# Performance work log

Measured on AMD Instinct MI355X. Metric: run time of the kernel, lower is better.

## Reference

```python
import jax, jax.numpy as jnp
import numpy as np

MARGIN = 0.2
NEG_SENTINEL = -1e30


def setup_inputs() -> dict:
    key = jax.random.key(0)
    k1, k2 = jax.random.split(key)
    batch_reprs = jax.random.normal(k1, (4096, 128), dtype=jnp.float32)
    batch_labels = jax.random.randint(k2, (4096,), 0, 512, dtype=jnp.int64 if jax.config.jax_enable_x64 else jnp.int32)
    return {"batch_reprs": batch_reprs, "batch_labels": batch_labels}


def _loss(batch_reprs, batch_labels):
    # class match matrix (self-similarity kept, as in original)
    match = (batch_labels[:, None] == batch_labels[None, :]).astype(batch_reprs.dtype)  # [B,B]

    # pairwise euclidean distance (squared=False), sim = -dist
    sq = jnp.sum(batch_reprs * batch_reprs, axis=1)
    d2 = jnp.maximum(sq[:, None] + sq[None, :] - 2.0 * (batch_reprs @ batch_reprs.T), 0.0)
    zero = (d2 == 0.0).astype(batch_reprs.dtype)
    dist = jnp.sqrt(d2 + zero * 1e-16) * (1.0 - zero)
    sim_hat = -dist + (1.0 - match) * MARGIN  # use_margin=True

    # rank positions via double argsort (descending)
    order = jnp.argsort(-sim_hat, axis=1)
    rank = jnp.argsort(order, axis=1).astype(sim_hat.dtype) + 1.0  # [B,B], 1-based ranks

    k = jnp.sum(match, axis=1, keepdims=True)                      # n_pos per row, [B,1]
    fp = (match < 1.0) & (rank <= k)                               # false positives
    fp_num = jnp.sum(fp, axis=1, keepdims=True).astype(sim_hat.dtype)
    fn = (match > 0.0) & (rank > k)                                # false negatives

    n = sim_hat.shape[1]
    # per-row top-(fp_num) false negatives by sim_hat, vectorized via masked sort
    fn_scores = jnp.where(fn, sim_hat, NEG_SENTINEL)
    idx = jnp.argsort(-fn_scores, axis=1)
    fn_sorted = jnp.take_along_axis(sim_hat, idx, axis=1)
    fn_ranks = jnp.take_along_axis(rank, idx, axis=1)
    fn_mask_sorted = jnp.take_along_axis(fn, idx, axis=1)
    sel = (jnp.arange(n)[None, :] < fp_num) & fn_mask_sorted       # top fp_num entries

    # weighted margins (rows with fp_num==0 contribute 0 automatically)
    fp_term = jnp.sum(jnp.where(fp, sim_hat * (0.5 + (k - rank + 1.0) / k * 0.5), 0.0))
    fn_term = jnp.sum(jnp.where(sel, fn_sorted * (0.5 + (fn_ranks - k) / (n - k) * 0.5), 0.0))
    return fp_term - fn_term


def reference(batch_reprs, batch_labels):
    return _loss(batch_reprs, batch_labels)
```

## Files before the change

kernel.cpp:

```cpp
#include <hip/hip_runtime.h>
#include <cstdint>
#include <cstddef>

#define B 4096
#define D 128
#define MARGIN_F 0.2f
#define CW 256
#define ROWS 16
#define SSTR 4104

typedef short bf16x8 __attribute__((ext_vector_type(8)));
typedef float f32x4 __attribute__((ext_vector_type(4)));
typedef uint32_t u32x4 __attribute__((ext_vector_type(4)));

__device__ __forceinline__ uint32_t xform_key(float f) {
    uint32_t u = __float_as_uint(f);
    return u ^ (uint32_t)((((int32_t)u) >> 31) | 0x80000000);
}
__device__ __forceinline__ float unxform16(uint32_t k16) {
    uint32_t u = k16 << 16;
    u = (u & 0x80000000u) ? (u ^ 0x80000000u) : ~u;
    return __uint_as_float(u);
}
__device__ __forceinline__ unsigned short f2bf(float f) {
    uint32_t u = __float_as_uint(f);
    return (unsigned short)((u + 0x7FFFu + ((u >> 16) & 1u)) >> 16);
}

__global__ __launch_bounds__(256) void prep_kernel(const float* __restrict__ R,
                                                   float* __restrict__ sq,
                                                   unsigned short* __restrict__ Rb,
                                                   float* __restrict__ out) {
    if (blockIdx.x == 0 && threadIdx.x == 0) out[0] = 0.0f;
    int wave = threadIdx.x >> 6;
    int lane = threadIdx.x & 63;
    int row  = blockIdx.x * 4 + wave;
    const float2* R2 = (const float2*)R + (size_t)row * (D / 2);
    float2 v = R2[lane];
    ushort2 o; o.x = f2bf(v.x); o.y = f2bf(v.y);
    *(ushort2*)(Rb + (size_t)row * D + lane * 2) = o;
    float s = v.x * v.x + v.y * v.y;
#pragma unroll
    for (int off = 32; off > 0; off >>= 1) s += __shfl_down(s, off);
    if (lane == 0) sq[row] = s;
}

__global__ __launch_bounds__(512) void fused_loss(const unsigned short* __restrict__ Rb,
                                                  const float* __restrict__ sq,
                                                  const int* __restrict__ labels,
                                                  float* __restrict__ out) {
    __shared__ unsigned short S[ROWS * SSTR];
    __shared__ uint32_t cand_c[ROWS][CW];
    __shared__ int cnt[ROWS];

    const int tid  = threadIdx.x;
    const int wid  = tid >> 6, lane = tid & 63;
    const int q    = lane >> 4, t = lane & 15;
    const int r0   = blockIdx.x * ROWS;

    {
        uint32_t* cz = &cand_c[0][0];
#pragma unroll
        for (int c = 0; c < (ROWS * CW) / 512; ++c)
            cz[tid + c * 512] = 0u;
    }
    if (tid < ROWS) cnt[tid] = 0;

    bf16x8 af[4];
    const unsigned short* baseA = Rb + (size_t)(r0 + t) * D + q * 8;
#pragma unroll
    for (int kq = 0; kq < 4; ++kq)
        af[kq] = *(const bf16x8*)(baseA + kq * 32);

    float sqa[4]; int la[4];
#pragma unroll
    for (int rr = 0; rr < 4; ++rr) {
        sqa[rr] = sq[r0 + q * 4 + rr];
        la[rr]  = labels[r0 + q * 4 + rr];
    }

    for (int i = 0; i < 32; ++i) {
        const int jt  = wid * 32 + i;
        const int col = jt * 16 + t;
        const unsigned short* baseB = Rb + (size_t)col * D + q * 8;
        bf16x8 bfr[4];
#pragma unroll
        for (int kq = 0; kq < 4; ++kq)
            bfr[kq] = *(const bf16x8*)(baseB + kq * 32);
        f32x4 acc = (f32x4)0.0f;
#pragma unroll
        for (int kq = 0; kq < 4; ++kq)
            acc = __builtin_amdgcn_mfma_f32_16x16x32_bf16(af[kq], bfr[kq], acc, 0, 0, 0);

        const float sqc = sq[col];
        const int   lc  = labels[col];
#pragma unroll
        for (int rr = 0; rr < 4; ++rr) {
            float g  = acc[rr];
            float d2 = fmaxf(sqa[rr] + sqc - 2.0f * g, 0.0f);
            float dist = (d2 > 0.0f) ? sqrtf(d2) : 0.0f;
            float s = -dist + ((la[rr] == lc) ? 0.0f : MARGIN_F);
            uint32_t key = xform_key(s);
            S[(q * 4 + rr) * SSTR + col] = (unsigned short)((key + 0x8000u) >> 16);
        }
    }
    __syncthreads();

    float facc = 0.0f;
    const int4* lv = (const int4*)labels;

    for (int rr2 = 0; rr2 < 2; ++rr2) {
        const int row  = wid * 2 + rr2;
        const int grow = r0 + row;
        const int li   = labels[grow];

        uint64_t mbits = 0;
        uint32_t t1 = 0, t2 = 0;

        {
            u32x4 kv[8];
#pragma unroll
            for (int qq = 0; qq < 8; ++qq)
                kv[qq] = *(u32x4*)(&S[row * SSTR + (qq * 64 + lane) * 8]);

#pragma unroll
            for (int qq = 0; qq < 8; ++qq) {
                const int lb = (qq * 64 + lane) * 2;
                int4 la4 = lv[lb], lc4 = lv[lb + 1];
                uint32_t u[8] = {kv[qq].x & 0xFFFFu, kv[qq].x >> 16,
                                 kv[qq].y & 0xFFFFu, kv[qq].y >> 16,
                                 kv[qq].z & 0xFFFFu, kv[qq].z >> 16,
                                 kv[qq].w & 0xFFFFu, kv[qq].w >> 16};
#pragma unroll
                for (int c = 0; c < 8; ++c) {
                    uint32_t mn = min(t1, u[c]);
                    t1 = max(t1, u[c]);
                    t2 = max(t2, mn);
                }
                mbits |= (uint64_t)(la4.x == li) << (qq * 8 + 0);
                mbits |= (uint64_t)(la4.y == li) << (qq * 8 + 1);
                mbits |= (uint64_t)(la4.z == li) << (qq * 8 + 2);
                mbits |= (uint64_t)(la4.w == li) << (qq * 8 + 3);
                mbits |= (uint64_t)(lc4.x == li) << (qq * 8 + 4);
                mbits |= (uint64_t)(lc4.y == li) << (qq * 8 + 5);
                mbits |= (uint64_t)(lc4.z == li) << (qq * 8 + 6);
                mbits |= (uint64_t)(lc4.w == li) << (qq * 8 + 7);
            }

            int kloc = __popcll(mbits);
#pragma unroll
            for (int off = 32; off > 0; off >>= 1) kloc += __shfl_xor(kloc, off);
            const int k0 = kloc;

            const int kneed = min(k0, 128);
            uint32_t T = 0;
#pragma unroll
            for (int b = 15; b >= 0; --b) {
                uint32_t g = T | (1u << b);
                int c = __popcll(__ballot(t1 >= g)) + __popcll(__ballot(t2 >= g));
                if (c >= kneed) T = g;
            }
            t1 = T;
            t2 = (uint32_t)k0;

#pragma unroll
            for (int qq = 0; qq < 8; ++qq) {
                uint32_t u[8] = {kv[qq].x & 0xFFFFu, kv[qq].x >> 16,
                                 kv[qq].y & 0xFFFFu, kv[qq].y >> 16,
                                 kv[qq].z & 0xFFFFu, kv[qq].z >> 16,
                                 kv[qq].w & 0xFFFFu, kv[qq].w >> 16};
                int jb = (qq * 64 + lane) * 8;
#pragma unroll
                for (int c = 0; c < 8; ++c) {
                    int e = qq * 8 + c;
                    uint32_t m = (uint32_t)((mbits >> e) & 1);
                    if (u[c] >= t1 || m) {
                        int p = atomicAdd(&cnt[row], 1);
                        if (p < CW)
                            cand_c[row][p] = (u[c] << 12) | (uint32_t)(4095 - (jb + c)) | (m << 31);
                    }
                }
            }
        }

        const uint32_t T = t1;
        const int k = (int)t2;
        const float kf = (float)k;
        const uint32_t combT = T << 12;
        const int ncand = min(cnt[row], CW);

        uint32_t cr0 = cand_c[row][lane];
        uint32_t cr1 = cand_c[row][lane + 64];
        uint32_t cr2 = cand_c[row][lane + 128];
        uint32_t cr3 = cand_c[row][lane + 192];
        uint32_t mycomb[4] = {cr0 & 0x7FFFFFFFu, cr1 & 0x7FFFFFFFu,
                              cr2 & 0x7FFFFFFFu, cr3 & 0x7FFFFFFFu};
        int mym[4]  = {(int)(cr0 >> 31), (int)(cr1 >> 31),
                       (int)(cr2 >> 31), (int)(cr3 >> 31)};
        int myok[4] = {lane < ncand, lane + 64 < ncand,
                       lane + 128 < ncand, lane + 192 < ncand};
        int myc[4]  = {0, 0, 0, 0};

        const int npad = (ncand + 7) & ~7;
        for (int c0i = 0; c0i < npad; c0i += 8) {
            u32x4 a = *(const u32x4*)&cand_c[row][c0i];
            u32x4 b = *(const u32x4*)&cand_c[row][c0i + 4];
            uint32_t vv[8] = {a.x, a.y, a.z, a.w, b.x, b.y, b.z, b.w};
#pragma unroll
            for (int e = 0; e < 8; ++e) {
                uint32_t vm = vv[e] & 0x7FFFFFFFu;
#pragma unroll
                for (int j = 0; j < 4; ++j)
                    myc[j] += (vm > mycomb[j]) ? 1 : 0;
            }
        }

#pragma unroll
        for (int j = 0; j < 4; ++j) {
            if (myok[j] && mycomb[j] >= combT) {
                int rank = 1 + myc[j];
                float v = unxform16(mycomb[j] >> 12);
                if (!mym[j] && rank <= k)
                    facc += v * (0.5f + ((kf - (float)rank + 1.0f) / kf) * 0.5f);
                else if (mym[j] && rank > k)
                    facc -= v * (0.5f + (((float)rank - kf) / (float)(B - k)) * 0.5f);
            }
        }

        uint32_t p0 = 0xFFFFFFFFu, p1 = 0xFFFFFFFFu, p2 = 0xFFFFFFFFu, p3 = 0xFFFFFFFFu;

        auto flush4 = [&](int npv) {
            int c0 = 0, c1 = 0, c2 = 0, c3 = 0;
#pragma unroll
            for (int qq = 0; qq < 8; ++qq) {
                u32x4 kq = *(const u32x4*)(&S[row * SSTR + (qq * 64 + lane) * 8]);
                uint32_t u[8] = {kq.x & 0xFFFFu, kq.x >> 16,
                                 kq.y & 0xFFFFu, kq.y >> 16,
                                 kq.z & 0xFFFFu, kq.z >> 16,
                                 kq.w & 0xFFFFu, kq.w >> 16};
                int jb = (qq * 64 + lane) * 8;
#pragma unroll
                for (int cc = 0; cc < 8; ++cc) {
                    uint32_t ce = (u[cc] << 12) | (uint32_t)(4095 - (jb + cc));
                    c0 += (ce > p0) ? 1 : 0;  c1 += (ce > p1) ? 1 : 0;
                    c2 += (ce > p2) ? 1 : 0;  c3 += (ce > p3) ? 1 : 0;
                }
            }
#pragma unroll
            for (int off = 32; off > 0; off >>= 1) {
                c0 += __shfl_xor(c0, off); c1 += __shfl_xor(c1, off);
                c2 += __shfl_xor(c2, off); c3 += __shfl_xor(c3, off);
            }
            if (lane == 0) {
                if (npv > 0) facc -= unxform16(p0 >> 12) * (0.5f + (((float)(1 + c0) - kf) / (float)(B - k)) * 0.5f);
                if (npv > 1) facc -= unxform16(p1 >> 12) * (0.5f + (((float)(1 + c1) - kf) / (float)(B - k)) * 0.5f);
                if (npv > 2) facc -= unxform16(p2 >> 12) * (0.5f + (((float)(1 + c2) - kf) / (float)(B - k)) * 0.5f);
                if (npv > 3) facc -= unxform16(p3 >> 12) * (0.5f + (((float)(1 + c3) - kf) / (float)(B - k)) * 0.5f);
            }
            p0 = p1 = p2 = p3 = 0xFFFFFFFFu;
        };

        int np = 0;
#pragma unroll
        for (int j = 0; j < 4; ++j) {
            uint64_t mg = __ballot(myok[j] && mym[j] && (mycomb[j] < combT));
            while (mg) {
                int src = __ffsll((unsigned long long)mg) - 1;
                mg &= mg - 1;
                uint32_t pc;
                if (j == 0)      pc = __shfl(mycomb[0], src);
                else if (j == 1) pc = __shfl(mycomb[1], src);
                else if (j == 2) pc = __shfl(mycomb[2], src);
                else             pc = __shfl(mycomb[3], src);
                switch (np) {
                    case 0: p0 = pc; break; case 1: p1 = pc; break;
                    case 2: p2 = pc; break; default: p3 = pc; break;
                }
                ++np;
                if (np == 4) { flush4(4); np = 0; }
            }
        }
        if (np > 0) flush4(np);
    }

#pragma unroll
    for (int off = 32; off > 0; off >>= 1) facc += __shfl_xor(facc, off);
    if (lane == 0) atomicAdd(out, facc);
}

extern "C" void kernel_launch(void* const* d_in, const int* in_sizes, int n_in,
                              void* d_out, int out_size, void* d_ws, size_t ws_size,
                              hipStream_t stream) {
    const float* R      = (const float*)d_in[0];
    const int*   labels = (const int*)d_in[1];
    float* out = (float*)d_out;

    float*          sq = (float*)d_ws;
    unsigned short* Rb = (unsigned short*)((char*)d_ws + 16 * 1024);

    hipLaunchKernelGGL(prep_kernel, dim3(B / 4), dim3(256), 0, stream, R, sq, Rb, out);
    hipLaunchKernelGGL(fused_loss, dim3(B / ROWS), dim3(512), 0, stream,
                       Rb, sq, labels, out);
}
```

Baseline: 134.1 us.

## Prefetch B tiles, interleave two rows per wave, replace atomic compaction with prefix scan

The GEMM loop now software-prefetches the next column tile's bf16 fragments, squared norms and labels so their loads overlap the current MFMA and epilogue. The selection phase processes both of a wave's rows together to give more independent work per instruction. The shared-memory atomicAdd candidate compaction is replaced by a deterministic wave prefix-sum compaction. Row keys are kept in registers for the below-threshold pass instead of being reloaded from LDS, which raises register pressure and may cut occupancy.

```diff
diff --git a/kernel.cpp b/kernel.cpp
--- a/kernel.cpp
+++ b/kernel.cpp
@@ -51,7 +51,6 @@
                                                   float* __restrict__ out) {
     __shared__ unsigned short S[ROWS * SSTR];
     __shared__ uint32_t cand_c[ROWS][CW];
-    __shared__ int cnt[ROWS];
 
     const int tid  = threadIdx.x;
     const int wid  = tid >> 6, lane = tid & 63;
@@ -64,7 +63,6 @@
         for (int c = 0; c < (ROWS * CW) / 512; ++c)
             cz[tid + c * 512] = 0u;
     }
-    if (tid < ROWS) cnt[tid] = 0;
 
     bf16x8 af[4];
     const unsigned short* baseA = Rb + (size_t)(r0 + t) * D + q * 8;
@@ -79,29 +77,50 @@
         la[rr]  = labels[r0 + q * 4 + rr];
     }
 
-    for (int i = 0; i < 32; ++i) {
-        const int jt  = wid * 32 + i;
-        const int col = jt * 16 + t;
-        const unsigned short* baseB = Rb + (size_t)col * D + q * 8;
+    {
+        const int jt0 = wid * 32;
+        int col = jt0 * 16 + t;
         bf16x8 bfr[4];
-#pragma unroll
-        for (int kq = 0; kq < 4; ++kq)
-            bfr[kq] = *(const bf16x8*)(baseB + kq * 32);
-        f32x4 acc = (f32x4)0.0f;
-#pragma unroll
-        for (int kq = 0; kq < 4; ++kq)
-            acc = __builtin_amdgcn_mfma_f32_16x16x32_bf16(af[kq], bfr[kq], acc, 0, 0, 0);
-
-        const float sqc = sq[col];
-        const int   lc  = labels[col];
-#pragma unroll
-        for (int rr = 0; rr < 4; ++rr) {
-            float g  = acc[rr];
-            float d2 = fmaxf(sqa[rr] + sqc - 2.0f * g, 0.0f);
-            float dist = (d2 > 0.0f) ? sqrtf(d2) : 0.0f;
-            float s = -dist + ((la[rr] == lc) ? 0.0f : MARGIN_F);
-            uint32_t key = xform_key(s);
-            S[(q * 4 + rr) * SSTR + col] = (unsigned short)((key + 0x8000u) >> 16);
+        {
+            const unsigned short* baseB = Rb + (size_t)col * D + q * 8;
+#pragma unroll
+            for (int kq = 0; kq < 4; ++kq)
+                bfr[kq] = *(const bf16x8*)(baseB + kq * 32);
+        }
+        float sqc = sq[col];
+        int   lc  = labels[col];
+
+        for (int i = 0; i < 32; ++i) {
+            const int jn   = (i < 31) ? (jt0 + i + 1) : (jt0 + 31);
+            const int coln = jn * 16 + t;
+            bf16x8 bnx[4];
+            {
+                const unsigned short* baseB = Rb + (size_t)coln * D + q * 8;
+#pragma unroll
+                for (int kq = 0; kq < 4; ++kq)
+                    bnx[kq] = *(const bf16x8*)(baseB + kq * 32);
+            }
+            const float sqn = sq[coln];
+            const int   lcn = labels[coln];
+
+            f32x4 acc = (f32x4)0.0f;
+#pragma unroll
+            for (int kq = 0; kq < 4; ++kq)
+                acc = __builtin_amdgcn_mfma_f32_16x16x32_bf16(af[kq], bfr[kq], acc, 0, 0, 0);
+
+#pragma unroll
+            for (int rr = 0; rr < 4; ++rr) {
+                float g  = acc[rr];
+                float d2 = fmaxf(sqa[rr] + sqc - 2.0f * g, 0.0f);
+                float dist = (d2 > 0.0f) ? sqrtf(d2) : 0.0f;
+                float s = -dist + ((la[rr] == lc) ? 0.0f : MARGIN_F);
+                uint32_t key = xform_key(s);
+                S[(q * 4 + rr) * SSTR + col] = (unsigned short)((key + 0x8000u) >> 16);
+            }
+
+#pragma unroll
+            for (int kq = 0; kq < 4; ++kq) bfr[kq] = bnx[kq];
+            sqc = sqn; lc = lcn; col = coln;
         }
     }
     __syncthreads();
@@ -109,135 +128,222 @@
     float facc = 0.0f;
     const int4* lv = (const int4*)labels;
 
-    for (int rr2 = 0; rr2 < 2; ++rr2) {
-        const int row  = wid * 2 + rr2;
-        const int grow = r0 + row;
-        const int li   = labels[grow];
-
-        uint64_t mbits = 0;
-        uint32_t t1 = 0, t2 = 0;
-
-        {
-            u32x4 kv[8];
-#pragma unroll
-            for (int qq = 0; qq < 8; ++qq)
-                kv[qq] = *(u32x4*)(&S[row * SSTR + (qq * 64 + lane) * 8]);
-
-#pragma unroll
-            for (int qq = 0; qq < 8; ++qq) {
-                const int lb = (qq * 64 + lane) * 2;
-                int4 la4 = lv[lb], lc4 = lv[lb + 1];
-                uint32_t u[8] = {kv[qq].x & 0xFFFFu, kv[qq].x >> 16,
-                                 kv[qq].y & 0xFFFFu, kv[qq].y >> 16,
-                                 kv[qq].z & 0xFFFFu, kv[qq].z >> 16,
-                                 kv[qq].w & 0xFFFFu, kv[qq].w >> 16};
-#pragma unroll
-                for (int c = 0; c < 8; ++c) {
-                    uint32_t mn = min(t1, u[c]);
-                    t1 = max(t1, u[c]);
-                    t2 = max(t2, mn);
+    const int rA = wid * 2, rB = wid * 2 + 1;
+    const int liA = labels[r0 + rA];
+    const int liB = labels[r0 + rB];
+
+    u32x4 kvA[8], kvB[8];
+#pragma unroll
+    for (int qq = 0; qq < 8; ++qq) {
+        kvA[qq] = *(u32x4*)(&S[rA * SSTR + (qq * 64 + lane) * 8]);
+        kvB[qq] = *(u32x4*)(&S[rB * SSTR + (qq * 64 + lane) * 8]);
+    }
+
+    uint64_t mbA = 0, mbB = 0;
+    uint32_t t1A = 0, t2A = 0, t1B = 0, t2B = 0;
+
+#pragma unroll
+    for (int qq = 0; qq < 8; ++qq) {
+        const int lb = (qq * 64 + lane) * 2;
+        int4 la4 = lv[lb], lc4 = lv[lb + 1];
+        uint32_t uA[8] = {kvA[qq].x & 0xFFFFu, kvA[qq].x >> 16,
+                          kvA[qq].y & 0xFFFFu, kvA[qq].y >> 16,
+                          kvA[qq].z & 0xFFFFu, kvA[qq].z >> 16,
+                          kvA[qq].w & 0xFFFFu, kvA[qq].w >> 16};
+        uint32_t uB[8] = {kvB[qq].x & 0xFFFFu, kvB[qq].x >> 16,
+                          kvB[qq].y & 0xFFFFu, kvB[qq].y >> 16,
+                          kvB[qq].z & 0xFFFFu, kvB[qq].z >> 16,
+                          kvB[qq].w & 0xFFFFu, kvB[qq].w >> 16};
+#pragma unroll
+        for (int c = 0; c < 8; ++c) {
+            uint32_t mnA = min(t1A, uA[c]);
+            t1A = max(t1A, uA[c]);
+            t2A = max(t2A, mnA);
+            uint32_t mnB = min(t1B, uB[c]);
+            t1B = max(t1B, uB[c]);
+            t2B = max(t2B, mnB);
+        }
+        mbA |= (uint64_t)(la4.x == liA) << (qq * 8 + 0);
+        mbA |= (uint64_t)(la4.y == liA) << (qq * 8 + 1);
+        mbA |= (uint64_t)(la4.z == liA) << (qq * 8 + 2);
+        mbA |= (uint64_t)(la4.w == liA) << (qq * 8 + 3);
+        mbA |= (uint64_t)(lc4.x == liA) << (qq * 8 + 4);
+        mbA |= (uint64_t)(lc4.y == liA) << (qq * 8 + 5);
+        mbA |= (uint64_t)(lc4.z == liA) << (qq * 8 + 6);
+        mbA |= (uint64_t)(lc4.w == liA) << (qq * 8 + 7);
+        mbB |= (uint64_t)(la4.x == liB) << (qq * 8 + 0);
+        mbB |= (uint64_t)(la4.y == liB) << (qq * 8 + 1);
+        mbB |= (uint64_t)(la4.z == liB) << (qq * 8 + 2);
+        mbB |= (uint64_t)(la4.w == liB) << (qq * 8 + 3);
+        mbB |= (uint64_t)(lc4.x == liB) << (qq * 8 + 4);
+        mbB |= (uint64_t)(lc4.y == liB) << (qq * 8 + 5);
+        mbB |= (uint64_t)(lc4.z == liB) << (qq * 8 + 6);
+        mbB |= (uint64_t)(lc4.w == liB) << (qq * 8 + 7);
+    }
+
+    int klA = __popcll(mbA), klB = __popcll(mbB);
+#pragma unroll
+    for (int off = 32; off > 0; off >>= 1) {
+        klA += __shfl_xor(klA, off);
+        klB += __shfl_xor(klB, off);
+    }
+    const int kA = klA, kB = klB;
+    const float kfA = (float)kA, kfB = (float)kB;
+
+    const int kneedA = min(kA, 128), kneedB = min(kB, 128);
+    uint32_t TA = 0, TB = 0;
+#pragma unroll
+    for (int b = 15; b >= 0; --b) {
+        uint32_t gA = TA | (1u << b), gB = TB | (1u << b);
+        int cA = __popcll(__ballot(t1A >= gA)) + __popcll(__ballot(t2A >= gA));
+        int cB = __popcll(__ballot(t1B >= gB)) + __popcll(__ballot(t2B >= gB));
+        if (cA >= kneedA) TA = gA;
+        if (cB >= kneedB) TB = gB;
+    }
+    const uint32_t combTA = TA << 12, combTB = TB << 12;
+
+    uint64_t wmA = 0, wmB = 0;
+#pragma unroll
+    for (int qq = 0; qq < 8; ++qq) {
+        uint32_t uA[8] = {kvA[qq].x & 0xFFFFu, kvA[qq].x >> 16,
+                          kvA[qq].y & 0xFFFFu, kvA[qq].y >> 16,
+                          kvA[qq].z & 0xFFFFu, kvA[qq].z >> 16,
+                          kvA[qq].w & 0xFFFFu, kvA[qq].w >> 16};
+        uint32_t uB[8] = {kvB[qq].x & 0xFFFFu, kvB[qq].x >> 16,
+                          kvB[qq].y & 0xFFFFu, kvB[qq].y >> 16,
+                          kvB[qq].z & 0xFFFFu, kvB[qq].z >> 16,
+                          kvB[qq].w & 0xFFFFu, kvB[qq].w >> 16};
+#pragma unroll
+        for (int c = 0; c < 8; ++c) {
+            int e = qq * 8 + c;
+            uint32_t mA = (uint32_t)((mbA >> e) & 1);
+            uint32_t mB = (uint32_t)((mbB >> e) & 1);
+            wmA |= (uint64_t)((uA[c] >= TA) | mA) << e;
+            wmB |= (uint64_t)((uB[c] >= TB) | mB) << e;
+        }
+    }
+    int cwA = __popcll(wmA), cwB = __popcll(wmB);
+    int incA = cwA, incB = cwB;
+#pragma unroll
+    for (int off = 1; off < 64; off <<= 1) {
+        int vA = __shfl_up(incA, off);
+        int vB = __shfl_up(incB, off);
+        if (lane >= off) { incA += vA; incB += vB; }
+    }
+    int baseAi = incA - cwA, baseBi = incB - cwB;
+    const int totalA = __shfl(incA, 63), totalB = __shfl(incB, 63);
+
+#pragma unroll
+    for (int qq = 0; qq < 8; ++qq) {
+        uint32_t subA = (uint32_t)((wmA >> (qq * 8)) & 0xFFu);
+        uint32_t subB = (uint32_t)((wmB >> (qq * 8)) & 0xFFu);
+        uint32_t uA[8] = {kvA[qq].x & 0xFFFFu, kvA[qq].x >> 16,
+                          kvA[qq].y & 0xFFFFu, kvA[qq].y >> 16,
+                          kvA[qq].z & 0xFFFFu, kvA[qq].z >> 16,
+                          kvA[qq].w & 0xFFFFu, kvA[qq].w >> 16};
+        uint32_t uB[8] = {kvB[qq].x & 0xFFFFu, kvB[qq].x >> 16,
+                          kvB[qq].y & 0xFFFFu, kvB[qq].y >> 16,
+                          kvB[qq].z & 0xFFFFu, kvB[qq].z >> 16,
+                          kvB[qq].w & 0xFFFFu, kvB[qq].w >> 16};
+        int jb = (qq * 64 + lane) * 8;
+#pragma unroll
+        for (int c = 0; c < 8; ++c) {
+            if (subA & (1u << c)) {
+                if (baseAi < CW) {
+                    uint32_t m = (uint32_t)((mbA >> (qq * 8 + c)) & 1);
+                    cand_c[rA][baseAi] = (uA[c] << 12) | (uint32_t)(4095 - (jb + c)) | (m << 31);
                 }
-                mbits |= (uint64_t)(la4.x == li) << (qq * 8 + 0);
-                mbits |= (uint64_t)(la4.y == li) << (qq * 8 + 1);
-                mbits |= (uint64_t)(la4.z == li) << (qq * 8 + 2);
-                mbits |= (uint64_t)(la4.w == li) << (qq * 8 + 3);
-                mbits |= (uint64_t)(lc4.x == li) << (qq * 8 + 4);
-                mbits |= (uint64_t)(lc4.y == li) << (qq * 8 + 5);
-                mbits |= (uint64_t)(lc4.z == li) << (qq * 8 + 6);
-                mbits |= (uint64_t)(lc4.w == li) << (qq * 8 + 7);
-            }
-
-            int kloc = __popcll(mbits);
-#pragma unroll
-            for (int off = 32; off > 0; off >>= 1) kloc += __shfl_xor(kloc, off);
-            const int k0 = kloc;
-
-            const int kneed = min(k0, 128);
-            uint32_t T = 0;
-#pragma unroll
-            for (int b = 15; b >= 0; --b) {
-                uint32_t g = T | (1u << b);
-                int c = __popcll(__ballot(t1 >= g)) + __popcll(__ballot(t2 >= g));
-                if (c >= kneed) T = g;
-            }
-            t1 = T;
-            t2 = (uint32_t)k0;
-
-#pragma unroll
-            for (int qq = 0; qq < 8; ++qq) {
-                uint32_t u[8] = {kv[qq].x & 0xFFFFu, kv[qq].x >> 16,
-                                 kv[qq].y & 0xFFFFu, kv[qq].y >> 16,
-                                 kv[qq].z & 0xFFFFu, kv[qq].z >> 16,
-                                 kv[qq].w & 0xFFFFu, kv[qq].w >> 16};
-                int jb = (qq * 64 + lane) * 8;
-#pragma unroll
-                for (int c = 0; c < 8; ++c) {
-                    int e = qq * 8 + c;
-                    uint32_t m = (uint32_t)((mbits >> e) & 1);
-                    if (u[c] >= t1 || m) {
-                        int p = atomicAdd(&cnt[row], 1);
-                        if (p < CW)
-                            cand_c[row][p] = (u[c] << 12) | (uint32_t)(4095 - (jb + c)) | (m << 31);
-                    }
+                ++baseAi;
+            }
+            if (subB & (1u << c)) {
+                if (baseBi < CW) {
+                    uint32_t m = (uint32_t)((mbB >> (qq * 8 + c)) & 1);
+                    cand_c[rB][baseBi] = (uB[c] << 12) | (uint32_t)(4095 - (jb + c)) | (m << 31);
                 }
-            }
-        }
-
-        const uint32_t T = t1;
-        const int k = (int)t2;
-        const float kf = (float)k;
-        const uint32_t combT = T << 12;
-        const int ncand = min(cnt[row], CW);
-
-        uint32_t cr0 = cand_c[row][lane];
-        uint32_t cr1 = cand_c[row][lane + 64];
-        uint32_t cr2 = cand_c[row][lane + 128];
-        uint32_t cr3 = cand_c[row][lane + 192];
-        uint32_t mycomb[4] = {cr0 & 0x7FFFFFFFu, cr1 & 0x7FFFFFFFu,
-                              cr2 & 0x7FFFFFFFu, cr3 & 0x7FFFFFFFu};
-        int mym[4]  = {(int)(cr0 >> 31), (int)(cr1 >> 31),
-                       (int)(cr2 >> 31), (int)(cr3 >> 31)};
-        int myok[4] = {lane < ncand, lane + 64 < ncand,
-                       lane + 128 < ncand, lane + 192 < ncand};
-        int myc[4]  = {0, 0, 0, 0};
-
-        const int npad = (ncand + 7) & ~7;
-        for (int c0i = 0; c0i < npad; c0i += 8) {
-            u32x4 a = *(const u32x4*)&cand_c[row][c0i];
-            u32x4 b = *(const u32x4*)&cand_c[row][c0i + 4];
+                ++baseBi;
+            }
+        }
+    }
+    const int ncandA = min(totalA, CW), ncandB = min(totalB, CW);
+
+    __builtin_amdgcn_s_waitcnt(0);
+
+    uint32_t crA0 = cand_c[rA][lane],        crB0 = cand_c[rB][lane];
+    uint32_t crA1 = cand_c[rA][lane + 64],   crB1 = cand_c[rB][lane + 64];
+    uint32_t crA2 = cand_c[rA][lane + 128],  crB2 = cand_c[rB][lane + 128];
+    uint32_t crA3 = cand_c[rA][lane + 192],  crB3 = cand_c[rB][lane + 192];
+    uint32_t mcA[4] = {crA0 & 0x7FFFFFFFu, crA1 & 0x7FFFFFFFu,
+                       crA2 & 0x7FFFFFFFu, crA3 & 0x7FFFFFFFu};
+    uint32_t mcB[4] = {crB0 & 0x7FFFFFFFu, crB1 & 0x7FFFFFFFu,
+                       crB2 & 0x7FFFFFFFu, crB3 & 0x7FFFFFFFu};
+    int mmA[4] = {(int)(crA0 >> 31), (int)(crA1 >> 31), (int)(crA2 >> 31), (int)(crA3 >> 31)};
+    int mmB[4] = {(int)(crB0 >> 31), (int)(crB1 >> 31), (int)(crB2 >> 31), (int)(crB3 >> 31)};
+    int okA[4] = {lane < ncandA, lane + 64 < ncandA, lane + 128 < ncandA, lane + 192 < ncandA};
+    int okB[4] = {lane < ncandB, lane + 64 < ncandB, lane + 128 < ncandB, lane + 192 < ncandB};
+    int cntA[4] = {0, 0, 0, 0}, cntB[4] = {0, 0, 0, 0};
+
+    const int npadA = (ncandA + 7) & ~7;
+    const int npadB = (ncandB + 7) & ~7;
+    const int npadM = npadA > npadB ? npadA : npadB;
+    for (int c0i = 0; c0i < npadM; c0i += 8) {
+        if (c0i < npadA) {
+            u32x4 a = *(const u32x4*)&cand_c[rA][c0i];
+            u32x4 b = *(const u32x4*)&cand_c[rA][c0i + 4];
             uint32_t vv[8] = {a.x, a.y, a.z, a.w, b.x, b.y, b.z, b.w};
 #pragma unroll
             for (int e = 0; e < 8; ++e) {
                 uint32_t vm = vv[e] & 0x7FFFFFFFu;
 #pragma unroll
                 for (int j = 0; j < 4; ++j)
-                    myc[j] += (vm > mycomb[j]) ? 1 : 0;
-            }
-        }
-
-#pragma unroll
-        for (int j = 0; j < 4; ++j) {
-            if (myok[j] && mycomb[j] >= combT) {
-                int rank = 1 + myc[j];
-                float v = unxform16(mycomb[j] >> 12);
-                if (!mym[j] && rank <= k)
-                    facc += v * (0.5f + ((kf - (float)rank + 1.0f) / kf) * 0.5f);
-                else if (mym[j] && rank > k)
-                    facc -= v * (0.5f + (((float)rank - kf) / (float)(B - k)) * 0.5f);
-            }
-        }
-
+                    cntA[j] += (vm > mcA[j]) ? 1 : 0;
+            }
+        }
+        if (c0i < npadB) {
+            u32x4 a = *(const u32x4*)&cand_c[rB][c0i];
+            u32x4 b = *(const u32x4*)&cand_c[rB][c0i + 4];
+            uint32_t vv[8] = {a.x, a.y, a.z, a.w, b.x, b.y, b.z, b.w};
+#pragma unroll
+            for (int e = 0; e < 8; ++e) {
+                uint32_t vm = vv[e] & 0x7FFFFFFFu;
+#pragma unroll
+                for (int j = 0; j < 4; ++j)
+                    cntB[j] += (vm > mcB[j]) ? 1 : 0;
+            }
+        }
+    }
+
+#pragma unroll
+    for (int j = 0; j < 4; ++j) {
+        if (okA[j] && mcA[j] >= combTA) {
+            int rank = 1 + cntA[j];
+            float v = unxform16(mcA[j] >> 12);
+            if (!mmA[j] && rank <= kA)
+                facc += v * (0.5f + ((kfA - (float)rank + 1.0f) / kfA) * 0.5f);
+            else if (mmA[j] && rank > kA)
+                facc -= v * (0.5f + (((float)rank - kfA) / (float)(B - kA)) * 0.5f);
+        }
+        if (okB[j] && mcB[j] >= combTB) {
+            int rank = 1 + cntB[j];
+            float v = unxform16(mcB[j] >> 12);
+            if (!mmB[j] && rank <= kB)
+                facc += v * (0.5f + ((kfB - (float)rank + 1.0f) / kfB) * 0.5f);
+            else if (mmB[j] && rank > kB)
+                facc -= v * (0.5f + (((float)rank - kfB) / (float)(B - kB)) * 0.5f);
+        }
+    }
+
+    auto below_t = [&](auto& kvr, const uint32_t* mcr, const int* mmr, const int* okr,
+                       uint32_t combTr, float kfr, int kr) {
         uint32_t p0 = 0xFFFFFFFFu, p1 = 0xFFFFFFFFu, p2 = 0xFFFFFFFFu, p3 = 0xFFFFFFFFu;
 
         auto flush4 = [&](int npv) {
             int c0 = 0, c1 = 0, c2 = 0, c3 = 0;
 #pragma unroll
             for (int qq = 0; qq < 8; ++qq) {
-                u32x4 kq = *(const u32x4*)(&S[row * SSTR + (qq * 64 + lane) * 8]);
-                uint32_t u[8] = {kq.x & 0xFFFFu, kq.x >> 16,
-                                 kq.y & 0xFFFFu, kq.y >> 16,
-                                 kq.z & 0xFFFFu, kq.z >> 16,
-                                 kq.w & 0xFFFFu, kq.w >> 16};
+                uint32_t u[8] = {kvr[qq].x & 0xFFFFu, kvr[qq].x >> 16,
+                                 kvr[qq].y & 0xFFFFu, kvr[qq].y >> 16,
+                                 kvr[qq].z & 0xFFFFu, kvr[qq].z >> 16,
+                                 kvr[qq].w & 0xFFFFu, kvr[qq].w >> 16};
                 int jb = (qq * 64 + lane) * 8;
 #pragma unroll
                 for (int cc = 0; cc < 8; ++cc) {
@@ -252,10 +358,10 @@
                 c2 += __shfl_xor(c2, off); c3 += __shfl_xor(c3, off);
             }
             if (lane == 0) {
-                if (npv > 0) facc -= unxform16(p0 >> 12) * (0.5f + (((float)(1 + c0) - kf) / (float)(B - k)) * 0.5f);
-                if (npv > 1) facc -= unxform16(p1 >> 12) * (0.5f + (((float)(1 + c1) - kf) / (float)(B - k)) * 0.5f);
-                if (npv > 2) facc -= unxform16(p2 >> 12) * (0.5f + (((float)(1 + c2) - kf) / (float)(B - k)) * 0.5f);
-                if (npv > 3) facc -= unxform16(p3 >> 12) * (0.5f + (((float)(1 + c3) - kf) / (float)(B - k)) * 0.5f);
+                if (npv > 0) facc -= unxform16(p0 >> 12) * (0.5f + (((float)(1 + c0) - kfr) / (float)(B - kr)) * 0.5f);
+                if (npv > 1) facc -= unxform16(p1 >> 12) * (0.5f + (((float)(1 + c1) - kfr) / (float)(B - kr)) * 0.5f);
+                if (npv > 2) facc -= unxform16(p2 >> 12) * (0.5f + (((float)(1 + c2) - kfr) / (float)(B - kr)) * 0.5f);
+                if (npv > 3) facc -= unxform16(p3 >> 12) * (0.5f + (((float)(1 + c3) - kfr) / (float)(B - kr)) * 0.5f);
             }
             p0 = p1 = p2 = p3 = 0xFFFFFFFFu;
         };
@@ -263,15 +369,15 @@
         int np = 0;
 #pragma unroll
         for (int j = 0; j < 4; ++j) {
-            uint64_t mg = __ballot(myok[j] && mym[j] && (mycomb[j] < combT));
+            uint64_t mg = __ballot(okr[j] && mmr[j] && (mcr[j] < combTr));
             while (mg) {
                 int src = __ffsll((unsigned long long)mg) - 1;
                 mg &= mg - 1;
                 uint32_t pc;
-                if (j == 0)      pc = __shfl(mycomb[0], src);
-                else if (j == 1) pc = __shfl(mycomb[1], src);
-                else if (j == 2) pc = __shfl(mycomb[2], src);
-                else             pc = __shfl(mycomb[3], src);
+                if (j == 0)      pc = __shfl(mcr[0], src);
+                else if (j == 1) pc = __shfl(mcr[1], src);
+                else if (j == 2) pc = __shfl(mcr[2], src);
+                else             pc = __shfl(mcr[3], src);
                 switch (np) {
                     case 0: p0 = pc; break; case 1: p1 = pc; break;
                     case 2: p2 = pc; break; default: p3 = pc; break;
@@ -281,7 +387,10 @@
             }
         }
         if (np > 0) flush4(np);
-    }
+    };
+
+    below_t(kvA, mcA, mmA, okA, combTA, kfA, kA);
+    below_t(kvB, mcB, mmB, okB, combTB, kfB, kB);
 
 #pragma unroll
     for (int off = 32; off > 0; off >>= 1) facc += __shfl_xor(facc, off);
```

Result: no change. 133.0 us, median of 2 (-0.8%).
